# Performance work log

Measured on AMD Instinct MI355X. Metric: run time of the kernel, lower is better.

The kernel has to match this reference:

```python
import jax, jax.numpy as jnp
import numpy as np

B, C, H, W = 8, 128, 64, 64


def setup_inputs() -> dict:
    key = jax.random.key(0)
    ks = jax.random.split(key, 7)
    query_img = jax.random.normal(ks[0], (B, C, H, W), dtype=jnp.float32)
    key_img = jax.random.normal(ks[1], (B, C, H, W), dtype=jnp.float32)
    value_img = jax.random.normal(ks[2], (B, C, H, W), dtype=jnp.float32)
    # 1x1 conv weights == dense [out, in] matrices (kaiming-ish scale)
    scale = 1.0 / np.sqrt(C)
    Wq = jax.random.normal(ks[3], (C, C), dtype=jnp.float32) * scale
    bq = jax.random.normal(ks[4], (C,), dtype=jnp.float32) * scale
    Wk = jax.random.normal(ks[5], (C, C), dtype=jnp.float32) * scale
    bk = jax.random.normal(ks[6], (C,), dtype=jnp.float32) * scale
    return {"query_img": query_img, "key_img": key_img, "value_img": value_img,
            "Wq": Wq, "bq": bq, "Wk": Wk, "bk": bk}


def reference(query_img, key_img, value_img, Wq, bq, Wk, bk):
    b, c, h, w = query_img.shape
    hw = h * w
    # 1x1 convs as GEMMs -> token-major layout (b, hw, c_out)
    q = jnp.einsum('bchw,oc->bhwo', query_img, Wq).reshape(b, hw, -1) + bq
    k = jnp.einsum('bchw,oc->bohw', key_img, Wk).reshape(b, -1, hw) + bk[None, :, None]
    # scores scaled by sqrt(HW) (faithful: key.size(-1) == h*w in source)
    scores = jnp.einsum('bqc,bck->bqk', q, k) / jnp.sqrt(jnp.float32(hw))
    attn = jax.nn.softmax(scores, axis=-1)  # (b, hw, hw)
    v = value_img.reshape(b, c, hw).transpose(0, 2, 1)  # (b, hw, c)
    out = jnp.einsum('bqk,bkc->bqc', attn, v)  # (b, hw, c)
    out = out.transpose(0, 2, 1).reshape(b, -1, h, w)
    out = out + q.transpose(0, 2, 1).reshape(b, -1, h, w)  # residual from query proj
    return out
```

## Files before the change

kernel.cpp:

```cpp
#include <hip/hip_runtime.h>

#define BB 8
#define CC 128
#define SS 4096
#define KT 64
#define NSPLIT 2
#define HKV (SS / NSPLIT)
#define SCALE 0.015625f

typedef __attribute__((ext_vector_type(8))) short sh8;
typedef __attribute__((ext_vector_type(4))) float f32x4;

__device__ __forceinline__ float b2f(unsigned short u) {
    union { unsigned int i; float f; } x; x.i = ((unsigned int)u) << 16; return x.f;
}
__device__ __forceinline__ unsigned short f2b(float f) {
    union { float f; unsigned int i; } x; x.f = f;
    unsigned int r = x.i + 0x7fff + ((x.i >> 16) & 1);
    return (unsigned short)(r >> 16);
}
__device__ __forceinline__ unsigned short rhu(float f) {
    union { float f; unsigned int i; } x; x.f = f;
    return (unsigned short)((x.i + 0x8000) >> 16);
}

__device__ __forceinline__ void dma16(const void* g, void* l) {
    __builtin_amdgcn_global_load_lds((const __attribute__((address_space(1))) void*)g,
                                     (__attribute__((address_space(3))) void*)l,
                                     16, 0, 0);
}

__global__ __launch_bounds__(256) void cvt_kernel(
    const float* __restrict__ vimg,
    const float* __restrict__ Wq, const float* __restrict__ Wk,
    const float* __restrict__ bq, const float* __restrict__ bk,
    unsigned short* __restrict__ Vbuf,
    unsigned short* __restrict__ Wqb, unsigned short* __restrict__ Wkb,
    unsigned short* __restrict__ bqb, unsigned short* __restrict__ bkb)
{
    const int bx = blockIdx.x, tid = threadIdx.x;
    if (bx < 512) {
        const size_t base = (size_t)bx * 8192 + tid * 4;
        #pragma unroll
        for (int it = 0; it < 8; ++it) {
            const size_t i = base + (size_t)it * 1024;
            float4 v = *(const float4*)(vimg + i);
            ushort4 o;
            o.x = f2b(v.x); o.y = f2b(v.y); o.z = f2b(v.z); o.w = f2b(v.w);
            *(ushort4*)(Vbuf + i) = o;
        }
    } else {
        const int w = bx - 512;
        for (int e = w * 256 + tid; e < 33024; e += 2048) {
            float v; unsigned short* dst;
            if (e < 16384)      { v = Wq[e];         dst = Wqb + e; }
            else if (e < 32768) { v = Wk[e - 16384]; dst = Wkb + (e - 16384); }
            else if (e < 32896) { v = bq[e - 32768]; dst = bqb + (e - 32768); }
            else                { v = bk[e - 32896]; dst = bkb + (e - 32896); }
            *dst = f2b(v);
        }
    }
}

__global__ __launch_bounds__(256) void proj_kernel(
    const float* __restrict__ qimg, const float* __restrict__ kimg,
    const unsigned short* __restrict__ Wqb, const unsigned short* __restrict__ Wkb,
    const unsigned short* __restrict__ bqb, const unsigned short* __restrict__ bkb,
    unsigned short* __restrict__ Qbuf, unsigned short* __restrict__ Kbuf)
{
    __shared__ float ilds[128 * 69];

    const int z = blockIdx.z;
    const float* img = (z == 0) ? qimg : kimg;
    const unsigned short* Wb = (z == 0) ? Wqb : Wkb;
    const unsigned short* bias = (z == 0) ? bqb : bkb;
    unsigned short* outTok = (z == 0) ? Qbuf : Kbuf;

    const int tid  = threadIdx.x;
    const int wave = tid >> 6;
    const int lane = tid & 63;
    const int l15  = lane & 15;
    const int quad = lane >> 4;
    const int b     = blockIdx.y;
    const int stile = blockIdx.x;

    const float* gbase = img + (size_t)b * CC * SS + stile * 64;
    #pragma unroll
    for (int i = 0; i < 8; ++i) {
        const int l = tid + 256 * i;
        const int row = l >> 4, col = (l & 15) * 4;
        float4 v = *(const float4*)(gbase + (size_t)row * SS + col);
        float* d = ilds + row * 69 + col;
        d[0] = v.x; d[1] = v.y; d[2] = v.z; d[3] = v.w;
    }
    __syncthreads();

    const int tcol = wave * 16 + l15;
    sh8 a[4];
    #pragma unroll
    for (int kk = 0; kk < 4; ++kk)
        #pragma unroll
        for (int j = 0; j < 8; ++j)
            a[kk][j] = (short)rhu(ilds[(32 * kk + quad * 8 + j) * 69 + tcol]);

    f32x4 acc[8];
    #pragma unroll
    for (int nt = 0; nt < 8; ++nt) acc[nt] = (f32x4){0.f, 0.f, 0.f, 0.f};

    #pragma unroll
    for (int nt = 0; nt < 8; ++nt) {
        const unsigned short* wp = Wb + (size_t)(16 * nt + l15) * CC + quad * 8;
        #pragma unroll
        for (int kk = 0; kk < 4; ++kk) {
            sh8 bf = *(const sh8*)(wp + 32 * kk);
            acc[nt] = __builtin_amdgcn_mfma_f32_16x16x32_bf16(a[kk], bf, acc[nt], 0, 0, 0);
        }
    }

    #pragma unroll
    for (int nt = 0; nt < 8; ++nt) {
        const int o = 16 * nt + l15;
        const float bv = b2f(bias[o]);
        #pragma unroll
        for (int r = 0; r < 4; ++r) {
            const int s = stile * 64 + wave * 16 + quad * 4 + r;
            outTok[((size_t)b * SS + s) * CC + o] = f2b(acc[nt][r] + bv);
        }
    }
}

__global__ __launch_bounds__(256, 2) void attn_kernel(
    const unsigned short* __restrict__ Qbuf,
    const unsigned short* __restrict__ Kbuf,
    const unsigned short* __restrict__ Vbuf,
    unsigned short* __restrict__ Opart,
    float* __restrict__ Lsum)
{
    __shared__ __align__(16) unsigned char smem[65536];
    unsigned char* vb = smem + 32768;

    const int tid  = threadIdx.x;
    const int wave = tid >> 6;
    const int lane = tid & 63;
    const int l15  = lane & 15;
    const int quad = lane >> 4;
    const int wgid = blockIdx.x;
    const int b    = wgid & 7;
    const int half = (wgid >> 3) & 1;
    const int qt   = wgid >> 4;
    const int qbase = qt * 128 + wave * 32;
    const int tok0  = half * HKV;

    unsigned char* pw = smem + 49152 + wave * 4096;

    const unsigned short* kbp = Kbuf + (size_t)b * SS * CC;
    const unsigned short* vbp = Vbuf + (size_t)b * CC * SS;

    sh8 aq[2][4];
    #pragma unroll
    for (int m = 0; m < 2; ++m) {
        const unsigned short* qp = Qbuf + ((size_t)b * SS + qbase + m * 16 + l15) * CC + quad * 8;
        #pragma unroll
        for (int kk = 0; kk < 4; ++kk) aq[m][kk] = *(const sh8*)(qp + 32 * kk);
    }

    int kGO[4], vGO[4];
    #pragma unroll
    for (int j = 0; j < 4; ++j) {
        const int krow = wave * 16 + j * 4 + (lane >> 4);
        kGO[j] = krow * 256 + (((lane & 15) ^ (krow & 7)) << 4);
        const int vrow = (wave * 4 + j) * 8 + (lane >> 3);
        vGO[j] = vrow * 8192 + (((lane & 7) ^ ((lane >> 3) & 7)) << 4);
    }

    f32x4 oacc[2][8];
    #pragma unroll
    for (int m = 0; m < 2; ++m)
        #pragma unroll
        for (int ct = 0; ct < 8; ++ct) oacc[m][ct] = (f32x4){0.f, 0.f, 0.f, 0.f};
    float lsum[2][4] = {{0.f, 0.f, 0.f, 0.f}, {0.f, 0.f, 0.f, 0.f}};

    {
        const char* gk = (const char*)kbp + (size_t)tok0 * 256;
        const char* gv = (const char*)vbp + (size_t)tok0 * 2;
        #pragma unroll
        for (int j = 0; j < 4; ++j) {
            dma16(gk + kGO[j], smem + (wave * 4 + j) * 1024);
            dma16(gv + vGO[j], vb + (wave * 4 + j) * 1024);
        }
    }

    for (int it = 0; it < HKV / KT; ++it) {
        unsigned char* kb = smem + ((it & 1) << 14);

        __syncthreads();

        if (it + 1 < HKV / KT) {
            const char* gk = (const char*)kbp + (size_t)(tok0 + (it + 1) * KT) * 256;
            unsigned char* kbn = smem + (((it + 1) & 1) << 14);
            #pragma unroll
            for (int j = 0; j < 4; ++j) dma16(gk + kGO[j], kbn + (wave * 4 + j) * 1024);
        }

        f32x4 sacc[2][4];
        #pragma unroll
        for (int m = 0; m < 2; ++m)
            #pragma unroll
            for (int n = 0; n < 4; ++n) sacc[m][n] = (f32x4){0.f, 0.f, 0.f, 0.f};
        __builtin_amdgcn_s_setprio(1);
        #pragma unroll
        for (int n = 0; n < 4; ++n) {
            #pragma unroll
            for (int kk = 0; kk < 4; ++kk) {
                sh8 kf = *(const sh8*)(kb + (16 * n + l15) * 256
                                          + (((4 * kk + quad) ^ (l15 & 7)) << 4));
                sacc[0][n] = __builtin_amdgcn_mfma_f32_16x16x32_bf16(aq[0][kk], kf, sacc[0][n], 0, 0, 0);
                sacc[1][n] = __builtin_amdgcn_mfma_f32_16x16x32_bf16(aq[1][kk], kf, sacc[1][n], 0, 0, 0);
            }
        }
        __builtin_amdgcn_s_setprio(0);

        #pragma unroll
        for (int m = 0; m < 2; ++m)
            #pragma unroll
            for (int n = 0; n < 4; ++n)
                #pragma unroll
                for (int r = 0; r < 4; ++r) {
                    float p = __expf(sacc[m][n][r] * SCALE);
                    lsum[m][r] += p;
                    const int row = m * 16 + quad * 4 + r, col = 16 * n + l15;
                    *(unsigned short*)(pw + row * 128
                                       + (((col >> 3) ^ (row & 7)) << 4)
                                       + (col & 7) * 2) = rhu(p);
                }

        {
            sh8 ap0 = *(const sh8*)(pw + l15 * 128 + ((quad ^ (l15 & 7)) << 4));
            sh8 ap1 = *(const sh8*)(pw + (16 + l15) * 128 + ((quad ^ (l15 & 7)) << 4));
            __builtin_amdgcn_s_setprio(1);
            #pragma unroll
            for (int ct = 0; ct < 8; ++ct) {
                sh8 bv = *(const sh8*)(vb + (16 * ct + l15) * 128
                                          + ((quad ^ (l15 & 7)) << 4));
                oacc[0][ct] = __builtin_amdgcn_mfma_f32_16x16x32_bf16(ap0, bv, oacc[0][ct], 0, 0, 0);
                oacc[1][ct] = __builtin_amdgcn_mfma_f32_16x16x32_bf16(ap1, bv, oacc[1][ct], 0, 0, 0);
            }
            __builtin_amdgcn_s_setprio(0);
        }

        sh8 vv[8];
        #pragma unroll
        for (int ct = 0; ct < 8; ++ct)
            vv[ct] = *(const sh8*)(vb + (16 * ct + l15) * 128
                                      + (((4 + quad) ^ (l15 & 7)) << 4));

        __syncthreads();

        if (it + 1 < HKV / KT) {
            const char* gv = (const char*)vbp + (size_t)(tok0 + (it + 1) * KT) * 2;
            #pragma unroll
            for (int j = 0; j < 4; ++j) dma16(gv + vGO[j], vb + (wave * 4 + j) * 1024);
        }

        {
            sh8 ap0 = *(const sh8*)(pw + l15 * 128 + (((4 + quad) ^ (l15 & 7)) << 4));
            sh8 ap1 = *(const sh8*)(pw + (16 + l15) * 128 + (((4 + quad) ^ (l15 & 7)) << 4));
            __builtin_amdgcn_s_setprio(1);
            #pragma unroll
            for (int ct = 0; ct < 8; ++ct) {
                oacc[0][ct] = __builtin_amdgcn_mfma_f32_16x16x32_bf16(ap0, vv[ct], oacc[0][ct], 0, 0, 0);
                oacc[1][ct] = __builtin_amdgcn_mfma_f32_16x16x32_bf16(ap1, vv[ct], oacc[1][ct], 0, 0, 0);
            }
            __builtin_amdgcn_s_setprio(0);
        }
    }

    #pragma unroll
    for (int m = 0; m < 2; ++m)
        #pragma unroll
        for (int r = 0; r < 4; ++r) {
            float v = lsum[m][r];
            #pragma unroll
            for (int s = 8; s >= 1; s >>= 1) v += __shfl_xor(v, s, 64);
            lsum[m][r] = v;
        }

    unsigned short* oT = (unsigned short*)smem;
    #pragma unroll
    for (int m = 0; m < 2; ++m)
        #pragma unroll
        for (int ct = 0; ct < 8; ++ct) {
            const int c  = 16 * ct + l15;
            const int q0 = wave * 32 + m * 16 + quad * 4;
            ushort4 o;
            o.x = rhu(oacc[m][ct][0]); o.y = rhu(oacc[m][ct][1]);
            o.z = rhu(oacc[m][ct][2]); o.w = rhu(oacc[m][ct][3]);
            *(ushort4*)(oT + c * 136 + q0) = o;
        }

    if (l15 == 0) {
        float* lp = Lsum + ((size_t)half * BB + b) * SS + qt * 128;
        #pragma unroll
        for (int m = 0; m < 2; ++m)
            #pragma unroll
            for (int r = 0; r < 4; ++r)
                lp[wave * 32 + m * 16 + quad * 4 + r] = lsum[m][r];
    }
    __syncthreads();

    unsigned short* op = Opart + ((size_t)half * BB + b) * CC * SS + qt * 128;
    #pragma unroll
    for (int i = 0; i < 16; ++i) {
        const int idx = tid + 256 * i;
        const int c = idx >> 5, q4 = (idx & 31) * 4;
        *(ushort4*)(op + (size_t)c * SS + q4) = *(const ushort4*)(oT + c * 136 + q4);
    }
}

__global__ __launch_bounds__(256) void combine_kernel(
    const unsigned short* __restrict__ Qbuf,
    const unsigned short* __restrict__ Opart,
    const float* __restrict__ Lsum,
    float* __restrict__ out)
{
    const int b = blockIdx.y, st = blockIdx.x, tid = threadIdx.x;
    const int s0   = st * 64 + (tid & 15) * 4;
    const int coff = tid >> 4;

    float4 l0 = *(const float4*)(Lsum + (size_t)b * SS + s0);
    float4 l1 = *(const float4*)(Lsum + ((size_t)BB + b) * SS + s0);
    float rinv[4];
    rinv[0] = 1.f / (l0.x + l1.x); rinv[1] = 1.f / (l0.y + l1.y);
    rinv[2] = 1.f / (l0.z + l1.z); rinv[3] = 1.f / (l0.w + l1.w);

    const unsigned short* qb = Qbuf + (size_t)b * SS * CC;
    for (int c = coff; c < CC; c += 16) {
        const size_t po = ((size_t)b * CC + c) * SS + s0;
        ushort4 p0 = *(const ushort4*)(Opart + po);
        ushort4 p1 = *(const ushort4*)(Opart + (size_t)BB * CC * SS + po);
        float4 o;
        o.x = (b2f(p0.x) + b2f(p1.x)) * rinv[0] + b2f(qb[(size_t)(s0 + 0) * CC + c]);
        o.y = (b2f(p0.y) + b2f(p1.y)) * rinv[1] + b2f(qb[(size_t)(s0 + 1) * CC + c]);
        o.z = (b2f(p0.z) + b2f(p1.z)) * rinv[2] + b2f(qb[(size_t)(s0 + 2) * CC + c]);
        o.w = (b2f(p0.w) + b2f(p1.w)) * rinv[3] + b2f(qb[(size_t)(s0 + 3) * CC + c]);
        *(float4*)(out + po) = o;
    }
}

extern "C" void kernel_launch(void* const* d_in, const int* in_sizes, int n_in,
                              void* d_out, int out_size, void* d_ws, size_t ws_size,
                              hipStream_t stream) {
    const float* qimg = (const float*)d_in[0];
    const float* kimg = (const float*)d_in[1];
    const float* vimg = (const float*)d_in[2];
    const float* Wq   = (const float*)d_in[3];
    const float* bq   = (const float*)d_in[4];
    const float* Wk   = (const float*)d_in[5];
    const float* bk   = (const float*)d_in[6];
    float* out = (float*)d_out;

    unsigned short* Qbuf = (unsigned short*)d_ws;
    unsigned short* Kbuf = Qbuf + (size_t)BB * SS * CC;
    unsigned short* Vbuf = Kbuf + (size_t)BB * SS * CC;
    unsigned short* Wqb  = Vbuf + (size_t)BB * SS * CC;
    unsigned short* Wkb  = Wqb + CC * CC;
    unsigned short* bqb  = Wkb + CC * CC;
    unsigned short* bkb  = bqb + CC;
    unsigned short* Opart = bkb + CC;
    float* Lsum = (float*)(Opart + (size_t)NSPLIT * BB * CC * SS);

    cvt_kernel<<<dim3(520), 256, 0, stream>>>(vimg, Wq, Wk, bq, bk,
                                              Vbuf, Wqb, Wkb, bqb, bkb);
    proj_kernel<<<dim3(SS / 64, BB, 2), 256, 0, stream>>>(
        qimg, kimg, Wqb, Wkb, bqb, bkb, Qbuf, Kbuf);
    attn_kernel<<<dim3(NSPLIT * BB * (SS / 128)), 256, 0, stream>>>(
        Qbuf, Kbuf, Vbuf, Opart, Lsum);
    combine_kernel<<<dim3(SS / 64, BB), 256, 0, stream>>>(Qbuf, Opart, Lsum, out);
}
```

Before: 209.8 us.

## Keep P in registers via transposed QK MFMA and load V straight from global

The QK^T MFMA swaps its operands so the score tile comes out transposed, and the K rows are permuted in LDS so each lane's probabilities line up with the A-operand layout of the PV MFMA. The probabilities are packed to bf16 with v_cvt_pk_bf16_f32 and fed directly from registers, which removes the per-wave P round-trip through LDS. V fragments are now read directly from global memory into registers rather than staged through LDS, which drops the V DMA buffers and one __syncthreads per iteration and shrinks shared memory so more blocks can fit. The cost is that V global-load latency is now exposed inside the loop, and the row sums are reduced with a different shuffle pattern.

```diff
diff --git a/kernel.cpp b/kernel.cpp
--- a/kernel.cpp
+++ b/kernel.cpp
@@ -22,6 +22,11 @@
 __device__ __forceinline__ unsigned short rhu(float f) {
     union { float f; unsigned int i; } x; x.f = f;
     return (unsigned short)((x.i + 0x8000) >> 16);
+}
+__device__ __forceinline__ unsigned int cvtpk(float lo, float hi) {
+    unsigned int r;
+    asm("v_cvt_pk_bf16_f32 %0, %1, %2" : "=v"(r) : "v"(lo), "v"(hi));
+    return r;
 }
 
 __device__ __forceinline__ void dma16(const void* g, void* l) {
@@ -136,8 +141,7 @@
     unsigned short* __restrict__ Opart,
     float* __restrict__ Lsum)
 {
-    __shared__ __align__(16) unsigned char smem[65536];
-    unsigned char* vb = smem + 32768;
+    __shared__ __align__(16) unsigned char smem[34816];
 
     const int tid  = threadIdx.x;
     const int wave = tid >> 6;
@@ -151,8 +155,6 @@
     const int qbase = qt * 128 + wave * 32;
     const int tok0  = half * HKV;
 
-    unsigned char* pw = smem + 49152 + wave * 4096;
-
     const unsigned short* kbp = Kbuf + (size_t)b * SS * CC;
     const unsigned short* vbp = Vbuf + (size_t)b * CC * SS;
 
@@ -164,31 +166,35 @@
         for (int kk = 0; kk < 4; ++kk) aq[m][kk] = *(const sh8*)(qp + 32 * kk);
     }
 
-    int kGO[4], vGO[4];
+    int kGO[4];
     #pragma unroll
     for (int j = 0; j < 4; ++j) {
-        const int krow = wave * 16 + j * 4 + (lane >> 4);
-        kGO[j] = krow * 256 + (((lane & 15) ^ (krow & 7)) << 4);
-        const int vrow = (wave * 4 + j) * 8 + (lane >> 3);
-        vGO[j] = vrow * 8192 + (((lane & 7) ^ ((lane >> 3) & 7)) << 4);
-    }
+        const int krow = wave * 16 + j * 4 + quad;
+        const int sx = (krow & 3) | ((krow >> 1) & 4);
+        kGO[j] = krow * 256 + (((lane & 15) ^ sx) << 4);
+    }
+
+    int krb[4], krs[4];
+    #pragma unroll
+    for (int n = 0; n < 4; ++n) {
+        const int rowp = 32 * (n >> 1) + 8 * (l15 >> 2) + 4 * (n & 1) + (l15 & 3);
+        krb[n] = rowp * 256;
+        krs[n] = (rowp & 3) | ((rowp >> 1) & 4);
+    }
+
+    const unsigned short* vlane = vbp + (size_t)l15 * SS + quad * 8 + tok0;
 
     f32x4 oacc[2][8];
     #pragma unroll
     for (int m = 0; m < 2; ++m)
         #pragma unroll
         for (int ct = 0; ct < 8; ++ct) oacc[m][ct] = (f32x4){0.f, 0.f, 0.f, 0.f};
-    float lsum[2][4] = {{0.f, 0.f, 0.f, 0.f}, {0.f, 0.f, 0.f, 0.f}};
-
-    {
-        const char* gk = (const char*)kbp + (size_t)tok0 * 256;
-        const char* gv = (const char*)vbp + (size_t)tok0 * 2;
-        #pragma unroll
-        for (int j = 0; j < 4; ++j) {
-            dma16(gk + kGO[j], smem + (wave * 4 + j) * 1024);
-            dma16(gv + vGO[j], vb + (wave * 4 + j) * 1024);
-        }
-    }
+    float lsum[2] = {0.f, 0.f};
+
+    const char* gk0 = (const char*)kbp + (size_t)tok0 * 256;
+    #pragma unroll
+    for (int j = 0; j < 4; ++j)
+        dma16(gk0 + kGO[j], smem + (wave * 4 + j) * 1024);
 
     for (int it = 0; it < HKV / KT; ++it) {
         unsigned char* kb = smem + ((it & 1) << 14);
@@ -196,11 +202,17 @@
         __syncthreads();
 
         if (it + 1 < HKV / KT) {
-            const char* gk = (const char*)kbp + (size_t)(tok0 + (it + 1) * KT) * 256;
+            const char* gk = gk0 + (size_t)(it + 1) * KT * 256;
             unsigned char* kbn = smem + (((it + 1) & 1) << 14);
             #pragma unroll
             for (int j = 0; j < 4; ++j) dma16(gk + kGO[j], kbn + (wave * 4 + j) * 1024);
         }
+
+        const unsigned short* vit = vlane + it * KT;
+        sh8 vv0[8], vv1[8];
+        #pragma unroll
+        for (int ct = 0; ct < 8; ++ct)
+            vv0[ct] = *(const sh8*)(vit + (size_t)ct * 16 * SS);
 
         f32x4 sacc[2][4];
         #pragma unroll
@@ -212,78 +224,63 @@
         for (int n = 0; n < 4; ++n) {
             #pragma unroll
             for (int kk = 0; kk < 4; ++kk) {
-                sh8 kf = *(const sh8*)(kb + (16 * n + l15) * 256
-                                          + (((4 * kk + quad) ^ (l15 & 7)) << 4));
-                sacc[0][n] = __builtin_amdgcn_mfma_f32_16x16x32_bf16(aq[0][kk], kf, sacc[0][n], 0, 0, 0);
-                sacc[1][n] = __builtin_amdgcn_mfma_f32_16x16x32_bf16(aq[1][kk], kf, sacc[1][n], 0, 0, 0);
+                sh8 kf = *(const sh8*)(kb + krb[n] + (((4 * kk + quad) ^ krs[n]) << 4));
+                sacc[0][n] = __builtin_amdgcn_mfma_f32_16x16x32_bf16(kf, aq[0][kk], sacc[0][n], 0, 0, 0);
+                sacc[1][n] = __builtin_amdgcn_mfma_f32_16x16x32_bf16(kf, aq[1][kk], sacc[1][n], 0, 0, 0);
             }
         }
         __builtin_amdgcn_s_setprio(0);
 
         #pragma unroll
-        for (int m = 0; m < 2; ++m)
+        for (int ct = 0; ct < 8; ++ct)
+            vv1[ct] = *(const sh8*)(vit + (size_t)ct * 16 * SS + 32);
+
+        union { sh8 v; unsigned int d[4]; } pa[2][2];
+        #pragma unroll
+        for (int m = 0; m < 2; ++m) {
+            float p[4][4];
             #pragma unroll
             for (int n = 0; n < 4; ++n)
                 #pragma unroll
                 for (int r = 0; r < 4; ++r) {
-                    float p = __expf(sacc[m][n][r] * SCALE);
-                    lsum[m][r] += p;
-                    const int row = m * 16 + quad * 4 + r, col = 16 * n + l15;
-                    *(unsigned short*)(pw + row * 128
-                                       + (((col >> 3) ^ (row & 7)) << 4)
-                                       + (col & 7) * 2) = rhu(p);
+                    p[n][r] = __expf(sacc[m][n][r] * SCALE);
+                    lsum[m] += p[n][r];
                 }
-
-        {
-            sh8 ap0 = *(const sh8*)(pw + l15 * 128 + ((quad ^ (l15 & 7)) << 4));
-            sh8 ap1 = *(const sh8*)(pw + (16 + l15) * 128 + ((quad ^ (l15 & 7)) << 4));
-            __builtin_amdgcn_s_setprio(1);
-            #pragma unroll
-            for (int ct = 0; ct < 8; ++ct) {
-                sh8 bv = *(const sh8*)(vb + (16 * ct + l15) * 128
-                                          + ((quad ^ (l15 & 7)) << 4));
-                oacc[0][ct] = __builtin_amdgcn_mfma_f32_16x16x32_bf16(ap0, bv, oacc[0][ct], 0, 0, 0);
-                oacc[1][ct] = __builtin_amdgcn_mfma_f32_16x16x32_bf16(ap1, bv, oacc[1][ct], 0, 0, 0);
+            #pragma unroll
+            for (int kp = 0; kp < 2; ++kp) {
+                pa[m][kp].d[0] = cvtpk(p[2 * kp][0],     p[2 * kp][1]);
+                pa[m][kp].d[1] = cvtpk(p[2 * kp][2],     p[2 * kp][3]);
+                pa[m][kp].d[2] = cvtpk(p[2 * kp + 1][0], p[2 * kp + 1][1]);
+                pa[m][kp].d[3] = cvtpk(p[2 * kp + 1][2], p[2 * kp + 1][3]);
             }
-            __builtin_amdgcn_s_setprio(0);
-        }
-
-        sh8 vv[8];
-        #pragma unroll
-        for (int ct = 0; ct < 8; ++ct)
-            vv[ct] = *(const sh8*)(vb + (16 * ct + l15) * 128
-                                      + (((4 + quad) ^ (l15 & 7)) << 4));
-
-        __syncthreads();
-
-        if (it + 1 < HKV / KT) {
-            const char* gv = (const char*)vbp + (size_t)(tok0 + (it + 1) * KT) * 2;
-            #pragma unroll
-            for (int j = 0; j < 4; ++j) dma16(gv + vGO[j], vb + (wave * 4 + j) * 1024);
-        }
-
-        {
-            sh8 ap0 = *(const sh8*)(pw + l15 * 128 + (((4 + quad) ^ (l15 & 7)) << 4));
-            sh8 ap1 = *(const sh8*)(pw + (16 + l15) * 128 + (((4 + quad) ^ (l15 & 7)) << 4));
-            __builtin_amdgcn_s_setprio(1);
-            #pragma unroll
-            for (int ct = 0; ct < 8; ++ct) {
-                oacc[0][ct] = __builtin_amdgcn_mfma_f32_16x16x32_bf16(ap0, vv[ct], oacc[0][ct], 0, 0, 0);
-                oacc[1][ct] = __builtin_amdgcn_mfma_f32_16x16x32_bf16(ap1, vv[ct], oacc[1][ct], 0, 0, 0);
-            }
-            __builtin_amdgcn_s_setprio(0);
-        }
-    }
-
-    #pragma unroll
-    for (int m = 0; m < 2; ++m)
-        #pragma unroll
-        for (int r = 0; r < 4; ++r) {
-            float v = lsum[m][r];
-            #pragma unroll
-            for (int s = 8; s >= 1; s >>= 1) v += __shfl_xor(v, s, 64);
-            lsum[m][r] = v;
-        }
+        }
+
+        __builtin_amdgcn_s_setprio(1);
+        #pragma unroll
+        for (int ct = 0; ct < 8; ++ct) {
+            oacc[0][ct] = __builtin_amdgcn_mfma_f32_16x16x32_bf16(pa[0][0].v, vv0[ct], oacc[0][ct], 0, 0, 0);
+            oacc[1][ct] = __builtin_amdgcn_mfma_f32_16x16x32_bf16(pa[1][0].v, vv0[ct], oacc[1][ct], 0, 0, 0);
+        }
+        #pragma unroll
+        for (int ct = 0; ct < 8; ++ct) {
+            oacc[0][ct] = __builtin_amdgcn_mfma_f32_16x16x32_bf16(pa[0][1].v, vv1[ct], oacc[0][ct], 0, 0, 0);
+            oacc[1][ct] = __builtin_amdgcn_mfma_f32_16x16x32_bf16(pa[1][1].v, vv1[ct], oacc[1][ct], 0, 0, 0);
+        }
+        __builtin_amdgcn_s_setprio(0);
+    }
+
+    #pragma unroll
+    for (int m = 0; m < 2; ++m) {
+        lsum[m] += __shfl_xor(lsum[m], 16, 64);
+        lsum[m] += __shfl_xor(lsum[m], 32, 64);
+    }
+    if (quad == 0) {
+        float* lp = Lsum + ((size_t)half * BB + b) * SS + qbase;
+        lp[l15]      = lsum[0];
+        lp[16 + l15] = lsum[1];
+    }
+
+    __syncthreads();
 
     unsigned short* oT = (unsigned short*)smem;
     #pragma unroll
@@ -297,15 +294,6 @@
             o.z = rhu(oacc[m][ct][2]); o.w = rhu(oacc[m][ct][3]);
             *(ushort4*)(oT + c * 136 + q0) = o;
         }
-
-    if (l15 == 0) {
-        float* lp = Lsum + ((size_t)half * BB + b) * SS + qt * 128;
-        #pragma unroll
-        for (int m = 0; m < 2; ++m)
-            #pragma unroll
-            for (int r = 0; r < 4; ++r)
-                lp[wave * 32 + m * 16 + quad * 4 + r] = lsum[m][r];
-    }
     __syncthreads();
 
     unsigned short* op = Opart + ((size_t)half * BB + b) * CC * SS + qt * 128;
```

Result: slower. 260.1 us (+24.0%).
